# Optimization experiments

Measured on AMD Instinct MI355X. Metric: run time of the kernel, lower is better.

## Reference

```python
import jax, jax.numpy as jnp
import numpy as np

NUM_NODES = 500000
DIM = 128
BATCH = 131072
MOMENTUM = 0.9


def setup_inputs() -> dict:
    key = jax.random.key(0)
    ks = jax.random.split(key, 6)
    s = 1.0 / np.sqrt(DIM)
    return {
        "hidden": jax.random.normal(ks[0], (NUM_NODES, DIM), jnp.float32),
        "variance": jnp.ones((NUM_NODES, DIM), jnp.float32),
        "idx": jnp.arange(BATCH, dtype=jnp.int64 if jax.config.jax_enable_x64 else jnp.int32),
        "new_repr": jax.random.normal(ks[1], (BATCH, DIM), jnp.float32),
        "W_ih": jax.random.normal(ks[2], (3 * DIM, DIM), jnp.float32) * s,
        "W_hh": jax.random.normal(ks[3], (3 * DIM, DIM), jnp.float32) * s,
        "b_ih": jax.random.normal(ks[4], (3 * DIM,), jnp.float32) * s,
        "b_hh": jax.random.normal(ks[5], (3 * DIM,), jnp.float32) * s,
    }


def _gru_cell(x, h, W_ih, W_hh, b_ih, b_hh):
    # torch GRUCell gate layout: [reset | update | new], each of size DIM
    gi = x @ W_ih.T + b_ih          # [B, 3*DIM]
    gh = h @ W_hh.T + b_hh          # [B, 3*DIM]
    gi_r, gi_z, gi_n = jnp.split(gi, 3, axis=-1)
    gh_r, gh_z, gh_n = jnp.split(gh, 3, axis=-1)
    r = jax.nn.sigmoid(gi_r + gh_r)
    z = jax.nn.sigmoid(gi_z + gh_z)
    n = jnp.tanh(gi_n + r * gh_n)
    return (1.0 - z) * n + z * h


def reference(hidden, variance, idx, new_repr, W_ih, W_hh, b_ih, b_hh):
    h_prev = hidden[idx]                                   # gather [B, DIM]
    h_new = _gru_cell(new_repr, h_prev, W_ih, W_hh, b_ih, b_hh)
    delta = h_new - h_prev
    var_new = MOMENTUM * variance[idx] + (1.0 - MOMENTUM) * delta * delta
    hidden_out = hidden.at[idx].set(h_new)                 # scatter write
    variance_out = variance.at[idx].set(var_new)
    return jnp.stack([hidden_out, variance_out])           # [2, N, DIM]
```

## Files before the change

### kernel.cpp

```cpp
#include <hip/hip_runtime.h>
#include <hip/hip_bf16.h>
#include <cstdint>
#include <cstddef>

#define NUM_NODES 500000
#define DIM 128
#define BATCH 131072

typedef __attribute__((ext_vector_type(8))) short short8;
typedef __attribute__((ext_vector_type(4))) short short4_t;
typedef __attribute__((ext_vector_type(4))) float f32x4;

static __device__ __forceinline__ short f2bf(float f) {
    unsigned u = __builtin_bit_cast(unsigned, f);
    u += 0x7fffu + ((u >> 16) & 1u);
    return (short)(u >> 16);
}

__global__ void k_init(int* __restrict__ mask,
                       const float* __restrict__ Wih,
                       const float* __restrict__ Whh,
                       short* __restrict__ WbIH,
                       short* __restrict__ WbHH,
                       int do_mask) {
    int i = blockIdx.x * blockDim.x + threadIdx.x;
    if (do_mask && i < NUM_NODES) mask[i] = 0;
    if (i < 3 * DIM * DIM) {
        WbIH[i] = f2bf(Wih[i]);
        WbHH[i] = f2bf(Whh[i]);
    }
}

__global__ void k_scatter(int* __restrict__ mask, const int* __restrict__ idx) {
    int i = blockIdx.x * blockDim.x + threadIdx.x;
    if (i < BATCH) mask[idx[i]] = 1;
}

__global__ void k_copy(const float* __restrict__ hidden,
                       const float* __restrict__ variance,
                       const int* __restrict__ mask,
                       float* __restrict__ out0,
                       float* __restrict__ out1) {
    int gid = blockIdx.x * blockDim.x + threadIdx.x;
    int row = gid >> 5;
    int c4  = gid & 31;
    if (row >= NUM_NODES) return;
    if (mask && mask[row]) return;
    size_t off = (size_t)row * DIM + c4 * 4;
    *(f32x4*)(out0 + off) = *(const f32x4*)(hidden + off);
    *(f32x4*)(out1 + off) = *(const f32x4*)(variance + off);
}

__global__ void __launch_bounds__(512)
k_gru(const float* __restrict__ hidden,
      const float* __restrict__ variance,
      const int*   __restrict__ idx,
      const float* __restrict__ xg,
      const short* __restrict__ WbIH,
      const short* __restrict__ WbHH,
      const float* __restrict__ b_ih,
      const float* __restrict__ b_hh,
      float* __restrict__ out0,
      float* __restrict__ out1) {
    __shared__ short Xb[32][136];
    __shared__ short Hb[32][136];
    __shared__ float Hf[32][132];
    __shared__ int   nodeS[32];

    const int t  = threadIdx.x;
    const int rb = blockIdx.x * 32;

    for (int j = t; j < 1024; j += 512) {
        int row = j >> 5, c4 = j & 31;
        int node = idx[rb + row];
        f32x4 xv = *(const f32x4*)(xg + (size_t)(rb + row) * DIM + c4 * 4);
        f32x4 hv = *(const f32x4*)(hidden + (size_t)node * DIM + c4 * 4);
        short4_t xs, hs;
        xs.x = f2bf(xv.x); xs.y = f2bf(xv.y); xs.z = f2bf(xv.z); xs.w = f2bf(xv.w);
        hs.x = f2bf(hv.x); hs.y = f2bf(hv.y); hs.z = f2bf(hv.z); hs.w = f2bf(hv.w);
        *(short4_t*)&Xb[row][c4 * 4] = xs;
        *(short4_t*)&Hb[row][c4 * 4] = hs;
        *(f32x4*)&Hf[row][c4 * 4]    = hv;
    }
    if (t < 32) nodeS[t] = idx[rb + t];
    __syncthreads();

    const int w = t >> 6;
    const int l = t & 63;
    const int c = l & 15;
    const int g = l >> 4;

    f32x4 acc[2][3][2] = {};

    #pragma unroll
    for (int ks = 0; ks < 4; ++ks) {
        const int k0 = ks * 32 + g * 8;
        short8 a[2][2];
        a[0][0] = *(const short8*)&Xb[c][k0];
        a[1][0] = *(const short8*)&Xb[16 + c][k0];
        a[0][1] = *(const short8*)&Hb[c][k0];
        a[1][1] = *(const short8*)&Hb[16 + c][k0];
        #pragma unroll
        for (int th = 0; th < 3; ++th) {
            const int o = w * 16 + th * 128 + c;
            const short8 bi = *(const short8*)(WbIH + (size_t)o * DIM + k0);
            const short8 bh = *(const short8*)(WbHH + (size_t)o * DIM + k0);
            #pragma unroll
            for (int mt = 0; mt < 2; ++mt) {
                acc[mt][th][0] = __builtin_amdgcn_mfma_f32_16x16x32_bf16(a[mt][0], bi, acc[mt][th][0], 0, 0, 0);
                acc[mt][th][1] = __builtin_amdgcn_mfma_f32_16x16x32_bf16(a[mt][1], bh, acc[mt][th][1], 0, 0, 0);
            }
        }
    }

    const int d = w * 16 + c;
    const float bs_r = b_ih[d]       + b_hh[d];
    const float bs_z = b_ih[d + 128] + b_hh[d + 128];
    const float bi_n = b_ih[d + 256];
    const float bh_n = b_hh[d + 256];

    #pragma unroll
    for (int mt = 0; mt < 2; ++mt) {
        #pragma unroll
        for (int r = 0; r < 4; ++r) {
            const int m = mt * 16 + g * 4 + r;
            float s_r  = acc[mt][0][0][r] + acc[mt][0][1][r] + bs_r;
            float s_z  = acc[mt][1][0][r] + acc[mt][1][1][r] + bs_z;
            float gi_n = acc[mt][2][0][r] + bi_n;
            float gh_n = acc[mt][2][1][r] + bh_n;
            float rg = 1.f / (1.f + __expf(-s_r));
            float zg = 1.f / (1.f + __expf(-s_z));
            float n  = tanhf(gi_n + rg * gh_n);
            float h  = Hf[m][d];
            float hn = (1.f - zg) * n + zg * h;
            float dl = hn - h;
            int node = nodeS[m];
            size_t off = (size_t)node * DIM + d;
            float var = 0.9f * variance[off] + 0.1f * dl * dl;
            out0[off] = hn;
            out1[off] = var;
        }
    }
}

extern "C" void kernel_launch(void* const* d_in, const int* in_sizes, int n_in,
                              void* d_out, int out_size, void* d_ws, size_t ws_size,
                              hipStream_t stream) {
    const float* hidden   = (const float*)d_in[0];
    const float* variance = (const float*)d_in[1];
    const int*   idx      = (const int*)d_in[2];
    const float* x        = (const float*)d_in[3];
    const float* Wih      = (const float*)d_in[4];
    const float* Whh      = (const float*)d_in[5];
    const float* bih      = (const float*)d_in[6];
    const float* bhh      = (const float*)d_in[7];
    float* out0 = (float*)d_out;
    float* out1 = out0 + (size_t)NUM_NODES * DIM;

    const size_t maskBytes = (size_t)NUM_NODES * 4;
    const size_t wBytes    = (size_t)3 * DIM * DIM * 2;
    const bool   have_mask = ws_size >= maskBytes + 2 * wBytes;

    int*   mask = have_mask ? (int*)d_ws : nullptr;
    short* WbIH = have_mask ? (short*)((char*)d_ws + maskBytes) : (short*)d_ws;
    short* WbHH = WbIH + 3 * DIM * DIM;

    k_init<<<(NUM_NODES + 255) / 256, 256, 0, stream>>>(mask ? mask : (int*)d_ws,
                                                        Wih, Whh, WbIH, WbHH,
                                                        have_mask ? 1 : 0);
    if (have_mask)
        k_scatter<<<BATCH / 256, 256, 0, stream>>>(mask, idx);

    k_copy<<<((size_t)NUM_NODES * 32 + 255) / 256, 256, 0, stream>>>(
        hidden, variance, mask, out0, out1);

    k_gru<<<BATCH / 32, 512, 0, stream>>>(hidden, variance, idx, x,
                                          WbIH, WbHH, bih, bhh, out0, out1);
}
```

Measured before the change: 301.6 us.

## Fuse masked copy and GRU into one interleaved kernel with coalesced scatter

Merges the masked bulk copy and the GRU update into a single launch. GRU blocks are interleaved one in eight among copy blocks, so the compute-heavy and bandwidth-heavy work can overlap and one kernel boundary disappears. The GRU epilogue now stages new hidden values in shared memory and writes both outputs as coalesced float4 rows. Other changes: the mask shrinks to one byte per node, the copy uses nontemporal loads and stores, and tanh becomes an exp-based formula. This adds extra barriers and shared-memory reuse in the GRU path, and the tanh formula may differ slightly in accuracy.

```diff
diff --git a/kernel.cpp b/kernel.cpp
--- a/kernel.cpp
+++ b/kernel.cpp
@@ -6,6 +6,8 @@
 #define NUM_NODES 500000
 #define DIM 128
 #define BATCH 131072
+#define GRU_BLOCKS (BATCH / 32)
+#define COPY_BLOCKS ((NUM_NODES * 32 + 511) / 512)
 
 typedef __attribute__((ext_vector_type(8))) short short8;
 typedef __attribute__((ext_vector_type(4))) short short4_t;
@@ -17,7 +19,7 @@
     return (short)(u >> 16);
 }
 
-__global__ void k_init(int* __restrict__ mask,
+__global__ void k_init(unsigned char* __restrict__ mask,
                        const float* __restrict__ Wih,
                        const float* __restrict__ Whh,
                        short* __restrict__ WbIH,
@@ -31,48 +33,31 @@
     }
 }
 
-__global__ void k_scatter(int* __restrict__ mask, const int* __restrict__ idx) {
+__global__ void k_scatter(unsigned char* __restrict__ mask, const int* __restrict__ idx) {
     int i = blockIdx.x * blockDim.x + threadIdx.x;
     if (i < BATCH) mask[idx[i]] = 1;
 }
 
-__global__ void k_copy(const float* __restrict__ hidden,
-                       const float* __restrict__ variance,
-                       const int* __restrict__ mask,
-                       float* __restrict__ out0,
-                       float* __restrict__ out1) {
-    int gid = blockIdx.x * blockDim.x + threadIdx.x;
-    int row = gid >> 5;
-    int c4  = gid & 31;
-    if (row >= NUM_NODES) return;
-    if (mask && mask[row]) return;
-    size_t off = (size_t)row * DIM + c4 * 4;
-    *(f32x4*)(out0 + off) = *(const f32x4*)(hidden + off);
-    *(f32x4*)(out1 + off) = *(const f32x4*)(variance + off);
-}
-
-__global__ void __launch_bounds__(512)
-k_gru(const float* __restrict__ hidden,
-      const float* __restrict__ variance,
-      const int*   __restrict__ idx,
-      const float* __restrict__ xg,
-      const short* __restrict__ WbIH,
-      const short* __restrict__ WbHH,
-      const float* __restrict__ b_ih,
-      const float* __restrict__ b_hh,
-      float* __restrict__ out0,
-      float* __restrict__ out1) {
-    __shared__ short Xb[32][136];
-    __shared__ short Hb[32][136];
-    __shared__ float Hf[32][132];
-    __shared__ int   nodeS[32];
-
-    const int t  = threadIdx.x;
-    const int rb = blockIdx.x * 32;
+__device__ __forceinline__ void gru_body(
+        int g, int t, char* smem,
+        const float* __restrict__ hidden, const float* __restrict__ variance,
+        const int* __restrict__ idx, const float* __restrict__ xg,
+        const short* __restrict__ WbIH, const short* __restrict__ WbHH,
+        const float* __restrict__ b_ih, const float* __restrict__ b_hh,
+        float* __restrict__ out0, float* __restrict__ out1) {
+    short (*Xb)[136] = (short(*)[136])smem;
+    short (*Hb)[136] = (short(*)[136])(smem + 8704);
+    float (*Hf)[132] = (float(*)[132])(smem + 17408);
+    float (*Hn)[132] = (float(*)[132])smem;
+    int*   nodeS     = (int*)(smem + 34304);
+
+    const int rb = g * 32;
+    if (t < 32) nodeS[t] = idx[rb + t];
+    __syncthreads();
 
     for (int j = t; j < 1024; j += 512) {
         int row = j >> 5, c4 = j & 31;
-        int node = idx[rb + row];
+        int node = nodeS[row];
         f32x4 xv = *(const f32x4*)(xg + (size_t)(rb + row) * DIM + c4 * 4);
         f32x4 hv = *(const f32x4*)(hidden + (size_t)node * DIM + c4 * 4);
         short4_t xs, hs;
@@ -82,19 +67,18 @@
         *(short4_t*)&Hb[row][c4 * 4] = hs;
         *(f32x4*)&Hf[row][c4 * 4]    = hv;
     }
-    if (t < 32) nodeS[t] = idx[rb + t];
-    __syncthreads();
-
-    const int w = t >> 6;
-    const int l = t & 63;
-    const int c = l & 15;
-    const int g = l >> 4;
+    __syncthreads();
+
+    const int w  = t >> 6;
+    const int l  = t & 63;
+    const int c  = l & 15;
+    const int gq = l >> 4;
 
     f32x4 acc[2][3][2] = {};
 
     #pragma unroll
     for (int ks = 0; ks < 4; ++ks) {
-        const int k0 = ks * 32 + g * 8;
+        const int k0 = ks * 32 + gq * 8;
         short8 a[2][2];
         a[0][0] = *(const short8*)&Xb[c][k0];
         a[1][0] = *(const short8*)&Xb[16 + c][k0];
@@ -113,6 +97,8 @@
         }
     }
 
+    __syncthreads();
+
     const int d = w * 16 + c;
     const float bs_r = b_ih[d]       + b_hh[d];
     const float bs_z = b_ih[d + 128] + b_hh[d + 128];
@@ -123,23 +109,76 @@
     for (int mt = 0; mt < 2; ++mt) {
         #pragma unroll
         for (int r = 0; r < 4; ++r) {
-            const int m = mt * 16 + g * 4 + r;
+            const int m = mt * 16 + gq * 4 + r;
             float s_r  = acc[mt][0][0][r] + acc[mt][0][1][r] + bs_r;
             float s_z  = acc[mt][1][0][r] + acc[mt][1][1][r] + bs_z;
             float gi_n = acc[mt][2][0][r] + bi_n;
             float gh_n = acc[mt][2][1][r] + bh_n;
             float rg = 1.f / (1.f + __expf(-s_r));
             float zg = 1.f / (1.f + __expf(-s_z));
-            float n  = tanhf(gi_n + rg * gh_n);
+            float aa = gi_n + rg * gh_n;
+            float n  = 1.f - 2.f / (__expf(2.f * aa) + 1.f);
             float h  = Hf[m][d];
-            float hn = (1.f - zg) * n + zg * h;
-            float dl = hn - h;
-            int node = nodeS[m];
-            size_t off = (size_t)node * DIM + d;
-            float var = 0.9f * variance[off] + 0.1f * dl * dl;
-            out0[off] = hn;
-            out1[off] = var;
+            Hn[m][d] = (1.f - zg) * n + zg * h;
         }
+    }
+    __syncthreads();
+
+    for (int j = t; j < 1024; j += 512) {
+        int row = j >> 5, c4 = j & 31;
+        int node = nodeS[row];
+        size_t off = (size_t)node * DIM + c4 * 4;
+        f32x4 hn = *(f32x4*)&Hn[row][c4 * 4];
+        f32x4 h  = *(f32x4*)&Hf[row][c4 * 4];
+        f32x4 vv = *(const f32x4*)(variance + off);
+        f32x4 var;
+        var.x = 0.9f * vv.x + 0.1f * (hn.x - h.x) * (hn.x - h.x);
+        var.y = 0.9f * vv.y + 0.1f * (hn.y - h.y) * (hn.y - h.y);
+        var.z = 0.9f * vv.z + 0.1f * (hn.z - h.z) * (hn.z - h.z);
+        var.w = 0.9f * vv.w + 0.1f * (hn.w - h.w) * (hn.w - h.w);
+        *(f32x4*)(out0 + off) = hn;
+        *(f32x4*)(out1 + off) = var;
+    }
+}
+
+__device__ __forceinline__ void copy_body(
+        int cb, int t,
+        const float* __restrict__ hidden, const float* __restrict__ variance,
+        const unsigned char* __restrict__ mask,
+        float* __restrict__ out0, float* __restrict__ out1) {
+    int gid = cb * 512 + t;
+    int row = gid >> 5;
+    int c4  = gid & 31;
+    if (row >= NUM_NODES) return;
+    if (mask && mask[row]) return;
+    size_t off = (size_t)row * DIM + c4 * 4;
+    f32x4 a = __builtin_nontemporal_load((const f32x4*)(hidden + off));
+    f32x4 b = __builtin_nontemporal_load((const f32x4*)(variance + off));
+    __builtin_nontemporal_store(a, (f32x4*)(out0 + off));
+    __builtin_nontemporal_store(b, (f32x4*)(out1 + off));
+}
+
+__global__ void __launch_bounds__(512, 4)
+k_main(const float* __restrict__ hidden, const float* __restrict__ variance,
+       const int* __restrict__ idx, const float* __restrict__ xg,
+       const short* __restrict__ WbIH, const short* __restrict__ WbHH,
+       const float* __restrict__ b_ih, const float* __restrict__ b_hh,
+       const unsigned char* __restrict__ mask,
+       float* __restrict__ out0, float* __restrict__ out1, int mode) {
+    __shared__ __align__(16) char smem[34432];
+    const int b = blockIdx.x;
+    const int t = threadIdx.x;
+    if (mode == 1) { copy_body(b, t, hidden, variance, nullptr, out0, out1); return; }
+    if (mode == 2) {
+        gru_body(b, t, smem, hidden, variance, idx, xg, WbIH, WbHH, b_ih, b_hh, out0, out1);
+        return;
+    }
+    const bool isGru = ((b & 7) == 0) && ((b >> 3) < GRU_BLOCKS);
+    if (isGru) {
+        gru_body(b >> 3, t, smem, hidden, variance, idx, xg, WbIH, WbHH, b_ih, b_hh, out0, out1);
+    } else {
+        int nGruBefore = (b >> 3) < GRU_BLOCKS ? (b >> 3) + 1 : GRU_BLOCKS;
+        copy_body(b - nGruBefore, t, hidden, variance, mask, out0, out1);
     }
 }
 
@@ -157,23 +196,26 @@
     float* out0 = (float*)d_out;
     float* out1 = out0 + (size_t)NUM_NODES * DIM;
 
-    const size_t maskBytes = (size_t)NUM_NODES * 4;
+    const size_t maskBytes = (size_t)NUM_NODES;
     const size_t wBytes    = (size_t)3 * DIM * DIM * 2;
     const bool   have_mask = ws_size >= maskBytes + 2 * wBytes;
 
-    int*   mask = have_mask ? (int*)d_ws : nullptr;
-    short* WbIH = have_mask ? (short*)((char*)d_ws + maskBytes) : (short*)d_ws;
+    unsigned char* mask = have_mask ? (unsigned char*)d_ws : nullptr;
+    short* WbIH = have_mask ? (short*)((char*)d_ws + ((maskBytes + 15) & ~size_t(15)))
+                            : (short*)d_ws;
     short* WbHH = WbIH + 3 * DIM * DIM;
 
-    k_init<<<(NUM_NODES + 255) / 256, 256, 0, stream>>>(mask ? mask : (int*)d_ws,
-                                                        Wih, Whh, WbIH, WbHH,
-                                                        have_mask ? 1 : 0);
-    if (have_mask)
+    k_init<<<(NUM_NODES + 255) / 256, 256, 0, stream>>>(
+        mask ? mask : (unsigned char*)d_ws, Wih, Whh, WbIH, WbHH, have_mask ? 1 : 0);
+
+    if (have_mask) {
         k_scatter<<<BATCH / 256, 256, 0, stream>>>(mask, idx);
-
-    k_copy<<<((size_t)NUM_NODES * 32 + 255) / 256, 256, 0, stream>>>(
-        hidden, variance, mask, out0, out1);
-
-    k_gru<<<BATCH / 32, 512, 0, stream>>>(hidden, variance, idx, x,
-                                          WbIH, WbHH, bih, bhh, out0, out1);
-}
+        k_main<<<GRU_BLOCKS + COPY_BLOCKS, 512, 0, stream>>>(
+            hidden, variance, idx, x, WbIH, WbHH, bih, bhh, mask, out0, out1, 0);
+    } else {
+        k_main<<<COPY_BLOCKS, 512, 0, stream>>>(
+            hidden, variance, idx, x, WbIH, WbHH, bih, bhh, nullptr, out0, out1, 1);
+        k_main<<<GRU_BLOCKS, 512, 0, stream>>>(
+            hidden, variance, idx, x, WbIH, WbHH, bih, bhh, nullptr, out0, out1, 2);
+    }
+}
```

Result: slower. 1.090 ms (+261.3%).
